# Optimization experiments

Hardware: AMD Instinct MI355X
Metric: run time of the kernel (lower is better)

The kernel has to match this reference:

```python
import jax, jax.numpy as jnp
import numpy as np

GAMMA_EPS = 0.05
ALPHA_POS = 4.0
ALPHA_NEG = 1.0

N, D, K_CLUSTERS = 262144, 128, 256


def setup_inputs() -> dict:
    key = jax.random.key(0)
    k1, k2, k3 = jax.random.split(key, 3)
    Xemb = jax.random.normal(k1, (N, D), dtype=jnp.float32)
    scores = jax.random.normal(k2, (N, K_CLUSTERS), dtype=jnp.float32)
    labels = jax.random.randint(k3, (N,), 0, K_CLUSTERS, dtype=jnp.int64)
    h_bias = jnp.asarray(0.1, dtype=jnp.float32)  # nn.Parameter(init_bias)
    return {"Xemb": Xemb, "scores": scores, "labels": labels,
            "h_bias": h_bias, "K": K_CLUSTERS}


def _bcl_forward(Xemb, scores, h_bias, labels, K):
    # labels are uniform in [0, K), so sorted unique labels == arange(K)
    # and the loop's k-index equals the label itself (pos_idx = labels).
    bias = jax.nn.softplus(h_bias)
    pos_bias = bias
    neg_bias = 9.0 * bias + GAMMA_EPS

    # scatter-mean centroids per cluster, then L2-normalize each centroid
    sums = jax.ops.segment_sum(Xemb, labels, num_segments=K)          # [K, D]
    counts = jax.ops.segment_sum(jnp.ones((Xemb.shape[0],), Xemb.dtype),
                                 labels, num_segments=K)              # [K]
    centroids = sums / counts[:, None]
    centroids = centroids / jnp.linalg.norm(centroids, axis=1, keepdims=True)

    x2 = jnp.sum(Xemb * Xemb, axis=1, keepdims=True)                  # [N, 1]
    c2 = jnp.sum(centroids * centroids, axis=1)                       # [K]
    XC_dist = x2 + c2[None, :] - 2.0 * (Xemb @ centroids.T)           # [N, K]

    # positive distance: gather own-cluster column
    pos_distances = jnp.take_along_axis(XC_dist, labels[:, None], axis=1)[:, 0]
    pos_sample_loss = jax.nn.relu(pos_distances - pos_bias)

    # min over negative clusters (exclude own column)
    own = jax.nn.one_hot(labels, K, dtype=jnp.bool_)
    min_neg = jnp.min(jnp.where(own, jnp.inf, XC_dist), axis=1)
    neg_sample_loss = jax.nn.relu(neg_bias - min_neg)

    pos_loss = jnp.mean(pos_sample_loss) * ALPHA_POS
    neg_loss = jnp.mean(neg_sample_loss) * ALPHA_NEG
    return jnp.stack([pos_loss, neg_loss])  # [ctrd_pos, ctrd_neg]


def reference(Xemb, scores, labels, h_bias, K):
    return _bcl_forward(Xemb, scores, h_bias, labels, K)
```

## Files before the change

### kernel.cpp

```cpp
#include <hip/hip_runtime.h>
#include <hip/hip_bf16.h>

#define DD 128
#define KK 256
#define TS 128
#define ROWB 136
#define SPB1 1024

typedef __attribute__((ext_vector_type(8))) short short8;
typedef __attribute__((ext_vector_type(4))) float f32x4;

static __device__ __forceinline__ unsigned short f2bf(float f) {
    unsigned int u = __float_as_uint(f);
    return (unsigned short)((u + 0x7fffu + ((u >> 16) & 1u)) >> 16);
}
static __device__ __forceinline__ float bf2f(unsigned short h) {
    return __uint_as_float(((unsigned int)h) << 16);
}

template<int MODE>
__global__ __launch_bounds__(1024) void k_stage1_gather(
    const float* __restrict__ X, const int* __restrict__ labels,
    float* __restrict__ partial, unsigned int* __restrict__ Xbf)
{
    __shared__ int lab[SPB1];
    __shared__ int idx[SPB1];
    __shared__ int hist[KK];
    __shared__ int start[KK + 1];
    __shared__ int cursor[KK];

    const int tid  = threadIdx.x;
    const int lane = tid & 63;
    const int wave = tid >> 6;
    const int base = blockIdx.x * SPB1;

    if (tid < KK) hist[tid] = 0;
    __syncthreads();
    {
        const int l = labels[base + tid];
        lab[tid] = l;
        atomicAdd(&hist[l], 1);
    }
    __syncthreads();
    if (wave == 0) {
        const int h0 = hist[4*lane], h1 = hist[4*lane+1];
        const int h2 = hist[4*lane+2], h3 = hist[4*lane+3];
        const int s = h0 + h1 + h2 + h3;
        int t = s;
#pragma unroll
        for (int d = 1; d < 64; d <<= 1) { const int u = __shfl_up(t, d); if (lane >= d) t += u; }
        const int e = t - s;
        start[4*lane]   = e;
        start[4*lane+1] = e + h0;
        start[4*lane+2] = e + h0 + h1;
        start[4*lane+3] = e + h0 + h1 + h2;
        if (lane == 63) start[KK] = t;
    }
    __syncthreads();
    if (tid < KK) cursor[tid] = start[tid];
    __syncthreads();
    {
        const int pos = atomicAdd(&cursor[lab[tid]], 1);
        idx[pos] = tid;
    }
    __syncthreads();

    for (int c = wave; c < KK; c += 16) {
        const int s0 = start[c], s1 = start[c + 1];
        float2 acc = make_float2(0.f, 0.f);
        if (s1 > s0) {
            int n0 = idx[s0];
            float2 v = *(const float2*)(X + (size_t)(base + n0) * DD + 2 * lane);
            for (int i = s0 + 1; i < s1; ++i) {
                const int n1 = idx[i];
                const float2 v1 = *(const float2*)(X + (size_t)(base + n1) * DD + 2 * lane);
                acc.x += v.x; acc.y += v.y;
                if (MODE == 0)
                    Xbf[(size_t)(base + n0) * (DD / 2) + lane] =
                        ((unsigned)f2bf(v.y) << 16) | (unsigned)f2bf(v.x);
                n0 = n1; v = v1;
            }
            acc.x += v.x; acc.y += v.y;
            if (MODE == 0)
                Xbf[(size_t)(base + n0) * (DD / 2) + lane] =
                    ((unsigned)f2bf(v.y) << 16) | (unsigned)f2bf(v.x);
        }
        if (MODE == 2) {
            atomicAdd(&partial[(size_t)c * DD + 2 * lane],     acc.x);
            atomicAdd(&partial[(size_t)c * DD + 2 * lane + 1], acc.y);
        } else {
            *(float2*)(partial + ((size_t)blockIdx.x * KK + c) * DD + 2 * lane) = acc;
        }
    }
}

__global__ void k_stage2(const float* __restrict__ partial, int nparts,
                         unsigned short* __restrict__ centb)
{
    const int k = blockIdx.x;
    const int t = threadIdx.x;
    const int d = t & (DD - 1);
    const int slice = t >> 7;
    float s = 0.f;
    for (int b = slice; b < nparts; b += 4)
        s += partial[((size_t)b * KK + k) * DD + d];
    __shared__ float red[4][DD];
    red[slice][d] = s;
    __syncthreads();
    float v = 0.f;
    if (t < DD) v = red[0][d] + red[1][d] + red[2][d] + red[3][d];
    float sq = v * v;
#pragma unroll
    for (int m = 32; m > 0; m >>= 1) sq += __shfl_xor(sq, m);
    __shared__ float wsum[8];
    if ((t & 63) == 0) wsum[t >> 6] = sq;
    __syncthreads();
    if (t < DD) centb[k * DD + d] = f2bf(v * rsqrtf(wsum[0] + wsum[1]));
}

template<int BF16SRC>
__global__ __launch_bounds__(512, 1) void k_stage3(
    const float* __restrict__ Xf, const unsigned int* __restrict__ Xbf,
    const int* __restrict__ labels, const unsigned short* __restrict__ centb,
    const float* __restrict__ hbias, float* __restrict__ loss, int spb)
{
    __shared__ unsigned short Cl[KK * ROWB];
    __shared__ unsigned short Xl[TS * ROWB];
    __shared__ int   labs[TS];
    __shared__ float lred[16];

    const int tid = threadIdx.x;
    const float hb = *hbias;
    const float bias = (hb > 20.f) ? hb : log1pf(__expf(hb));
    const float pos_bias = bias;
    const float neg_bias = 9.f * bias + 0.05f;

    const uint4* csrc = (const uint4*)centb;
    for (int c = tid; c < KK * DD / 8; c += 512) {
        const int row = c >> 4;
        const int col = (c & 15) << 3;
        *(uint4*)(&Cl[row * ROWB + col]) = csrc[c];
    }

    const int lane = tid & 63;
    const int wave = tid >> 6;
    const int m15  = lane & 15;
    const int q    = lane >> 4;
    const int kq   = q << 3;
    const int base = blockIdx.x * spb;
    float pos_acc = 0.f, neg_acc = 0.f;

    for (int t0 = 0; t0 < spb; t0 += TS) {
        __syncthreads();
        if (BF16SRC) {
            const uint4* xsrc = (const uint4*)(Xbf + (size_t)(base + t0) * (DD / 2));
            for (int c = tid; c < TS * DD / 8; c += 512) {
                const int row = c >> 4;
                const int col = (c & 15) << 3;
                *(uint4*)(&Xl[row * ROWB + col]) = xsrc[c];
            }
        } else {
            const float4* xsrc = (const float4*)(Xf + (size_t)(base + t0) * DD);
            for (int c = tid; c < TS * DD / 4; c += 512) {
                const int row = c >> 5;
                const int col = (c & 31) << 2;
                const float4 v = xsrc[c];
                ushort4 pk = make_ushort4(f2bf(v.x), f2bf(v.y), f2bf(v.z), f2bf(v.w));
                *(ushort4*)(&Xl[row * ROWB + col]) = pk;
            }
        }
        if (tid < TS) labs[tid] = labels[base + t0 + tid];
        __syncthreads();

        short8 afrag[4];
        const int arow = (wave << 4) + m15;
#pragma unroll
        for (int s = 0; s < 4; ++s)
            afrag[s] = *(const short8*)(&Xl[arow * ROWB + (s << 5) + kq]);

        float x2p = 0.f;
#pragma unroll
        for (int s = 0; s < 4; ++s)
#pragma unroll
            for (int j = 0; j < 8; ++j) {
                const float e = bf2f((unsigned short)afrag[s][j]);
                x2p = fmaf(e, e, x2p);
            }
        x2p += __shfl_xor(x2p, 16);
        x2p += __shfl_xor(x2p, 32);

        f32x4 acc[16];
#pragma unroll
        for (int t = 0; t < 16; ++t) acc[t] = (f32x4){0.f, 0.f, 0.f, 0.f};
#pragma unroll
        for (int t = 0; t < 16; ++t) {
            const int brow = (t << 4) + m15;
#pragma unroll
            for (int s = 0; s < 4; ++s) {
                const short8 bfrag = *(const short8*)(&Cl[brow * ROWB + (s << 5) + kq]);
                acc[t] = __builtin_amdgcn_mfma_f32_16x16x32_bf16(afrag[s], bfrag, acc[t], 0, 0, 0);
            }
        }

#pragma unroll
        for (int r = 0; r < 4; ++r) {
            const int ml = (wave << 4) + (q << 2) + r;
            const int l  = labs[ml];
            const float x2 = __shfl(x2p, (q << 2) + r, 16);
            float posd = -1e30f, negd = -1e30f;
#pragma unroll
            for (int t = 0; t < 16; ++t) {
                const int cl = (t << 4) + m15;
                const float v = acc[t][r];
                const bool isp = (cl == l);
                posd = isp ? v : posd;
                negd = isp ? negd : fmaxf(negd, v);
            }
#pragma unroll
            for (int m = 1; m < 16; m <<= 1) {
                posd = fmaxf(posd, __shfl_xor(posd, m));
                negd = fmaxf(negd, __shfl_xor(negd, m));
            }
            if (m15 == 0) {
                const float pd = x2 + 1.0f - 2.f * posd;
                const float nd = x2 + 1.0f - 2.f * negd;
                pos_acc += fmaxf(pd - pos_bias, 0.f);
                neg_acc += fmaxf(neg_bias - nd, 0.f);
            }
        }
    }

#pragma unroll
    for (int m = 32; m > 0; m >>= 1) {
        pos_acc += __shfl_xor(pos_acc, m);
        neg_acc += __shfl_xor(neg_acc, m);
    }
    if (lane == 0) { lred[wave] = pos_acc; lred[8 + wave] = neg_acc; }
    __syncthreads();
    if (tid == 0) {
        float p = 0.f, n = 0.f;
#pragma unroll
        for (int w = 0; w < 8; ++w) { p += lred[w]; n += lred[8 + w]; }
        atomicAdd(&loss[0], p);
        atomicAdd(&loss[1], n);
    }
}

__global__ void k_final(const float* __restrict__ loss, float* __restrict__ out, float invN)
{
    if (threadIdx.x == 0) {
        out[0] = 4.0f * loss[0] * invN;
        out[1] = loss[1] * invN;
    }
}

extern "C" void kernel_launch(void* const* d_in, const int* in_sizes, int n_in,
                              void* d_out, int out_size, void* d_ws, size_t ws_size,
                              hipStream_t stream)
{
    const float* X      = (const float*)d_in[0];
    const int*   labels = (const int*)d_in[2];
    const float* hbias  = (const float*)d_in[3];
    float* out = (float*)d_out;
    const int N = in_sizes[0] / DD;
    const int G = N / SPB1;

    char* ws = (char*)d_ws;
    const size_t offC   = 256;
    const size_t offXbf = offC + (size_t)KK * DD * 2;
    const size_t szXbf  = (size_t)N * DD * 2;
    const size_t szPart = (size_t)G * KK * DD * 4;

    float*          loss  = (float*)ws;
    unsigned short* centb = (unsigned short*)(ws + offC);

    int mode;
    float* partial;
    unsigned int* Xbf = nullptr;
    if (ws_size >= offXbf + szXbf + szPart) {
        mode = 0; Xbf = (unsigned int*)(ws + offXbf);
        partial = (float*)(ws + offXbf + szXbf);
    } else if (ws_size >= offXbf + szPart) {
        mode = 1; partial = (float*)(ws + offXbf);
    } else {
        mode = 2; partial = (float*)(ws + offXbf);
    }
    const int nparts = (mode == 2) ? 1 : G;

    hipMemsetAsync(loss, 0, 2 * sizeof(float), stream);
    if (mode == 2) hipMemsetAsync(partial, 0, (size_t)KK * DD * 4, stream);

    if (mode == 0)      k_stage1_gather<0><<<G, 1024, 0, stream>>>(X, labels, partial, Xbf);
    else if (mode == 1) k_stage1_gather<1><<<G, 1024, 0, stream>>>(X, labels, partial, nullptr);
    else                k_stage1_gather<2><<<G, 1024, 0, stream>>>(X, labels, partial, nullptr);

    k_stage2<<<KK, 512, 0, stream>>>(partial, nparts, centb);

    if (mode == 0) k_stage3<1><<<G, 512, 0, stream>>>(nullptr, Xbf, labels, centb, hbias, loss, N / G);
    else           k_stage3<0><<<G, 512, 0, stream>>>(X, nullptr, labels, centb, hbias, loss, N / G);

    k_final<<<1, 64, 0, stream>>>(loss, out, 1.0f / (float)N);
}
```

Measured before the change: 482.4 us.

## Drop bf16 X scratch copy; convert fp32 in stage3 with 1024-thread blocks

Stage 1 no longer writes a bf16 copy of X to workspace, and stage 3 always reads fp32 X and converts it to bf16 while staging it into LDS. This removes the 64MB bf16 write and later reread, at the cost of reading 128MB of fp32 in stage 3. Stage 3 also moves to 1024-thread blocks with a 256-row tile, so 16 waves share the centroid tile in LDS. The launch-bounds hint is raised to 4, but LDS use (~138KB) probably still allows only one block per CU.

```diff
diff --git a/kernel.cpp b/kernel.cpp
--- a/kernel.cpp
+++ b/kernel.cpp
@@ -3,7 +3,7 @@
 
 #define DD 128
 #define KK 256
-#define TS 128
+#define TS 256
 #define ROWB 136
 #define SPB1 1024
 
@@ -21,7 +21,7 @@
 template<int MODE>
 __global__ __launch_bounds__(1024) void k_stage1_gather(
     const float* __restrict__ X, const int* __restrict__ labels,
-    float* __restrict__ partial, unsigned int* __restrict__ Xbf)
+    float* __restrict__ partial)
 {
     __shared__ int lab[SPB1];
     __shared__ int idx[SPB1];
@@ -75,15 +75,9 @@
                 const int n1 = idx[i];
                 const float2 v1 = *(const float2*)(X + (size_t)(base + n1) * DD + 2 * lane);
                 acc.x += v.x; acc.y += v.y;
-                if (MODE == 0)
-                    Xbf[(size_t)(base + n0) * (DD / 2) + lane] =
-                        ((unsigned)f2bf(v.y) << 16) | (unsigned)f2bf(v.x);
                 n0 = n1; v = v1;
             }
             acc.x += v.x; acc.y += v.y;
-            if (MODE == 0)
-                Xbf[(size_t)(base + n0) * (DD / 2) + lane] =
-                    ((unsigned)f2bf(v.y) << 16) | (unsigned)f2bf(v.x);
         }
         if (MODE == 2) {
             atomicAdd(&partial[(size_t)c * DD + 2 * lane],     acc.x);
@@ -118,16 +112,15 @@
     if (t < DD) centb[k * DD + d] = f2bf(v * rsqrtf(wsum[0] + wsum[1]));
 }
 
-template<int BF16SRC>
-__global__ __launch_bounds__(512, 1) void k_stage3(
-    const float* __restrict__ Xf, const unsigned int* __restrict__ Xbf,
-    const int* __restrict__ labels, const unsigned short* __restrict__ centb,
+__global__ __launch_bounds__(1024, 4) void k_stage3(
+    const float* __restrict__ Xf, const int* __restrict__ labels,
+    const unsigned short* __restrict__ centb,
     const float* __restrict__ hbias, float* __restrict__ loss, int spb)
 {
     __shared__ unsigned short Cl[KK * ROWB];
     __shared__ unsigned short Xl[TS * ROWB];
     __shared__ int   labs[TS];
-    __shared__ float lred[16];
+    __shared__ float lred[32];
 
     const int tid = threadIdx.x;
     const float hb = *hbias;
@@ -136,7 +129,7 @@
     const float neg_bias = 9.f * bias + 0.05f;
 
     const uint4* csrc = (const uint4*)centb;
-    for (int c = tid; c < KK * DD / 8; c += 512) {
+    for (int c = tid; c < KK * DD / 8; c += 1024) {
         const int row = c >> 4;
         const int col = (c & 15) << 3;
         *(uint4*)(&Cl[row * ROWB + col]) = csrc[c];
@@ -152,22 +145,13 @@
 
     for (int t0 = 0; t0 < spb; t0 += TS) {
         __syncthreads();
-        if (BF16SRC) {
-            const uint4* xsrc = (const uint4*)(Xbf + (size_t)(base + t0) * (DD / 2));
-            for (int c = tid; c < TS * DD / 8; c += 512) {
-                const int row = c >> 4;
-                const int col = (c & 15) << 3;
-                *(uint4*)(&Xl[row * ROWB + col]) = xsrc[c];
-            }
-        } else {
-            const float4* xsrc = (const float4*)(Xf + (size_t)(base + t0) * DD);
-            for (int c = tid; c < TS * DD / 4; c += 512) {
-                const int row = c >> 5;
-                const int col = (c & 31) << 2;
-                const float4 v = xsrc[c];
-                ushort4 pk = make_ushort4(f2bf(v.x), f2bf(v.y), f2bf(v.z), f2bf(v.w));
-                *(ushort4*)(&Xl[row * ROWB + col]) = pk;
-            }
+        const float4* xsrc = (const float4*)(Xf + (size_t)(base + t0) * DD);
+        for (int c = tid; c < TS * DD / 4; c += 1024) {
+            const int row = c >> 5;
+            const int col = (c & 31) << 2;
+            const float4 v = xsrc[c];
+            ushort4 pk = make_ushort4(f2bf(v.x), f2bf(v.y), f2bf(v.z), f2bf(v.w));
+            *(ushort4*)(&Xl[row * ROWB + col]) = pk;
         }
         if (tid < TS) labs[tid] = labels[base + t0 + tid];
         __syncthreads();
@@ -235,12 +219,12 @@
         pos_acc += __shfl_xor(pos_acc, m);
         neg_acc += __shfl_xor(neg_acc, m);
     }
-    if (lane == 0) { lred[wave] = pos_acc; lred[8 + wave] = neg_acc; }
+    if (lane == 0) { lred[wave] = pos_acc; lred[16 + wave] = neg_acc; }
     __syncthreads();
     if (tid == 0) {
         float p = 0.f, n = 0.f;
 #pragma unroll
-        for (int w = 0; w < 8; ++w) { p += lred[w]; n += lred[8 + w]; }
+        for (int w = 0; w < 16; ++w) { p += lred[w]; n += lred[16 + w]; }
         atomicAdd(&loss[0], p);
         atomicAdd(&loss[1], n);
     }
@@ -266,38 +250,26 @@
     const int G = N / SPB1;
 
     char* ws = (char*)d_ws;
-    const size_t offC   = 256;
-    const size_t offXbf = offC + (size_t)KK * DD * 2;
-    const size_t szXbf  = (size_t)N * DD * 2;
-    const size_t szPart = (size_t)G * KK * DD * 4;
-
-    float*          loss  = (float*)ws;
-    unsigned short* centb = (unsigned short*)(ws + offC);
-
-    int mode;
-    float* partial;
-    unsigned int* Xbf = nullptr;
-    if (ws_size >= offXbf + szXbf + szPart) {
-        mode = 0; Xbf = (unsigned int*)(ws + offXbf);
-        partial = (float*)(ws + offXbf + szXbf);
-    } else if (ws_size >= offXbf + szPart) {
-        mode = 1; partial = (float*)(ws + offXbf);
-    } else {
-        mode = 2; partial = (float*)(ws + offXbf);
-    }
+    const size_t offC    = 256;
+    const size_t offPart = offC + (size_t)KK * DD * 2;
+    const size_t szPart  = (size_t)G * KK * DD * 4;
+
+    float*          loss    = (float*)ws;
+    unsigned short* centb   = (unsigned short*)(ws + offC);
+    float*          partial = (float*)(ws + offPart);
+
+    const int mode   = (ws_size >= offPart + szPart) ? 0 : 2;
     const int nparts = (mode == 2) ? 1 : G;
 
     hipMemsetAsync(loss, 0, 2 * sizeof(float), stream);
     if (mode == 2) hipMemsetAsync(partial, 0, (size_t)KK * DD * 4, stream);
 
-    if (mode == 0)      k_stage1_gather<0><<<G, 1024, 0, stream>>>(X, labels, partial, Xbf);
-    else if (mode == 1) k_stage1_gather<1><<<G, 1024, 0, stream>>>(X, labels, partial, nullptr);
-    else                k_stage1_gather<2><<<G, 1024, 0, stream>>>(X, labels, partial, nullptr);
+    if (mode == 0) k_stage1_gather<0><<<G, 1024, 0, stream>>>(X, labels, partial);
+    else           k_stage1_gather<2><<<G, 1024, 0, stream>>>(X, labels, partial);
 
     k_stage2<<<KK, 512, 0, stream>>>(partial, nparts, centb);
 
-    if (mode == 0) k_stage3<1><<<G, 512, 0, stream>>>(nullptr, Xbf, labels, centb, hbias, loss, N / G);
-    else           k_stage3<0><<<G, 512, 0, stream>>>(X, nullptr, labels, centb, hbias, loss, N / G);
+    k_stage3<<<G, 1024, 0, stream>>>(X, labels, centb, hbias, loss, N / G);
 
     k_final<<<1, 64, 0, stream>>>(loss, out, 1.0f / (float)N);
 }
```

Result: no change. 479.9 us (-0.5%).
